# Kernel optimization log

Hardware: AMD Instinct MI355X
Metric: run time of the kernel (lower is better)

Reference implementation:

```python
import jax, jax.numpy as jnp
import numpy as np

D_MODEL = 256
NUM_HEADS = 8
HEAD_DIM = D_MODEL // NUM_HEADS


def setup_inputs() -> dict:
    key = jax.random.key(0)
    ks = jax.random.split(key, 16)
    B, C, H, W = 2, D_MODEL, 64, 64
    s = 0.02
    inp = {
        "query_feat": jax.random.normal(ks[0], (B, C, H, W), jnp.float32),
        "lateral_feat": jax.random.normal(ks[1], (B, C, H, W), jnp.float32),
        # 1x1 convs == per-pixel linear layers: weight (out, in), bias (out,)
        "Wq": jax.random.normal(ks[2], (C, C), jnp.float32) * s,
        "bq": jnp.zeros((C,), jnp.float32),
        "Wk": jax.random.normal(ks[3], (C, C), jnp.float32) * s,
        "bk": jnp.zeros((C,), jnp.float32),
        "Wv": jax.random.normal(ks[4], (C, C), jnp.float32) * s,
        "bv": jnp.zeros((C,), jnp.float32),
        "Wo": jax.random.normal(ks[5], (C, C), jnp.float32) * s,
        "bo": jnp.zeros((C,), jnp.float32),
        "W1": jax.random.normal(ks[6], (4 * C, C), jnp.float32) * s,
        "b1": jnp.zeros((4 * C,), jnp.float32),
        "W2": jax.random.normal(ks[7], (C, 4 * C), jnp.float32) * s,
        "b2": jnp.zeros((C,), jnp.float32),
    }
    return inp


def reference(query_feat, lateral_feat, Wq, bq, Wk, bk, Wv, bv, Wo, bo, W1, b1, W2, b2):
    B, C, H, W = query_feat.shape
    N = H * W
    h, d = NUM_HEADS, HEAD_DIM
    scale = d ** -0.5

    # (B,C,H,W) -> (B,N,C) tokens
    xq = query_feat.reshape(B, C, N).transpose(0, 2, 1)
    xl = lateral_feat.reshape(B, C, N).transpose(0, 2, 1)

    # 1x1-conv projections = dense per-token linear
    Q = (xq @ Wq.T + bq).reshape(B, N, h, d).transpose(0, 2, 1, 3)  # (B,h,N,d)
    K = (xl @ Wk.T + bk).reshape(B, N, h, d).transpose(0, 2, 1, 3)
    V = (xl @ Wv.T + bv).reshape(B, N, h, d).transpose(0, 2, 1, 3)

    scores = jnp.einsum("bhqd,bhkd->bhqk", Q, K) * scale  # (B,h,N,N)
    attn = jax.nn.softmax(scores, axis=-1)  # dropout = identity at inference
    out = jnp.einsum("bhqk,bhkd->bhqd", attn, V)  # (B,h,N,d)

    out = out.transpose(0, 2, 1, 3).reshape(B, N, C)  # (B,N,C)
    out = out @ Wo.T + bo
    out = out.transpose(0, 2, 1).reshape(B, C, H, W)
    out = out + query_feat  # residual

    # MLP on channels (1x1 convs + exact GELU)
    t = out.reshape(B, C, N).transpose(0, 2, 1)  # (B,N,C)
    hdn = jax.nn.gelu(t @ W1.T + b1, approximate=False)  # (B,N,4C)
    mlp = (hdn @ W2.T + b2).transpose(0, 2, 1).reshape(B, C, H, W)
    return out + mlp
```

## Files before the change

### kernel.cpp

```cpp
#include <hip/hip_runtime.h>
#include <math.h>

namespace {

constexpr int kB  = 2;
constexpr int kC  = 256;
constexpr int kN  = 4096;
constexpr int kHD = 32;
constexpr int kC4 = 1024;

typedef __attribute__((ext_vector_type(8))) short bf16x8;
typedef __attribute__((ext_vector_type(4))) float f32x4;
typedef __attribute__((ext_vector_type(16))) float f32x16;

__device__ __forceinline__ float gelu_exact(float x) {
  return 0.5f * x * (1.0f + erff(x * 0.70710678118654752f));
}

__device__ __forceinline__ unsigned short f2bf(float x) {
  unsigned u = __builtin_bit_cast(unsigned, x);
  u += 0x7FFFu + ((u >> 16) & 1u);
  return (unsigned short)(u >> 16);
}

__device__ __forceinline__ float bf2f(unsigned short us) {
  return __builtin_bit_cast(float, (unsigned)us << 16);
}

__device__ __forceinline__ float exp2_hw(float x) {
#if __has_builtin(__builtin_amdgcn_exp2f)
  return __builtin_amdgcn_exp2f(x);
#else
  float r;
  asm("v_exp_f32 %0, %1\n\ts_nop 1" : "=v"(r) : "v"(x));
  return r;
#endif
}

__device__ __forceinline__ unsigned cvt_pk_bf16(float lo, float hi) {
  unsigned r;
  asm("v_cvt_pk_bf16_f32 %0, %1, %2" : "=v"(r) : "v"(lo), "v"(hi));
  return r;
}

__global__ __launch_bounds__(256)
void convert_all(const float* __restrict__ qfeat, const float* __restrict__ lfeat,
                 const float* __restrict__ Wq, const float* __restrict__ Wk,
                 const float* __restrict__ Wv, const float* __restrict__ Wo,
                 const float* __restrict__ W1, const float* __restrict__ W2,
                 unsigned short* __restrict__ qtok, unsigned short* __restrict__ ltok,
                 unsigned short* __restrict__ wbf)
{
  __shared__ float Lds[32][36];
  const int z = blockIdx.z;
  const int t = threadIdx.x;
  if (z < 4) {
    const float* src = (z < kB) ? qfeat : lfeat;
    unsigned short* dst = (z < kB) ? qtok : ltok;
    const int b = z & 1;
    src += (size_t)b * kC * kN;
    dst += (size_t)b * kN * kC;
    const int n0 = blockIdx.x * 32, c0 = blockIdx.y * 32;
    const int r = t >> 3, q4 = (t & 7) * 4;
    {
      const float4 v = *(const float4*)&src[(size_t)(c0 + r) * kN + n0 + q4];
      Lds[r][q4 + 0] = v.x; Lds[r][q4 + 1] = v.y; Lds[r][q4 + 2] = v.z; Lds[r][q4 + 3] = v.w;
    }
    __syncthreads();
    ushort4 p;
    p.x = f2bf(Lds[q4 + 0][r]); p.y = f2bf(Lds[q4 + 1][r]);
    p.z = f2bf(Lds[q4 + 2][r]); p.w = f2bf(Lds[q4 + 3][r]);
    *(ushort4*)&dst[(size_t)(n0 + r) * kC + c0 + q4] = p;
  } else {
    const int wi = blockIdx.y * 128 + blockIdx.x;
    if (wi >= 768) return;
    const int i4 = wi * 1024 + t * 4;
    const float* s; int base;
    if      (i4 < 65536)  { s = Wq; base = 0; }
    else if (i4 < 131072) { s = Wk; base = 65536; }
    else if (i4 < 196608) { s = Wv; base = 131072; }
    else if (i4 < 262144) { s = Wo; base = 196608; }
    else if (i4 < 524288) { s = W1; base = 262144; }
    else                  { s = W2; base = 524288; }
    const float4 v = *(const float4*)&s[i4 - base];
    ushort4 p;
    p.x = f2bf(v.x); p.y = f2bf(v.y); p.z = f2bf(v.z); p.w = f2bf(v.w);
    *(ushort4*)&wbf[i4] = p;
  }
}

__global__ __launch_bounds__(256)
void gemm_qkv(const unsigned short* __restrict__ wbf,
              const unsigned short* __restrict__ qtok,
              const unsigned short* __restrict__ ltok,
              const float* __restrict__ bq, const float* __restrict__ bk,
              const float* __restrict__ bv,
              unsigned short* __restrict__ qout, unsigned short* __restrict__ kout,
              unsigned short* __restrict__ vout, float qscale)
{
  __shared__ unsigned short Wlds[2][64 * 64];
  __shared__ unsigned short Xlds[2][64 * 64];

  const int z = blockIdx.z;
  const bool isQ = blockIdx.y < 4;
  const int m0 = (isQ ? blockIdx.y : blockIdx.y - 4) * 64;
  const unsigned short* Wb = isQ ? wbf : (wbf + 65536);
  const unsigned short* Xt = (isQ ? qtok : ltok) + (size_t)z * kN * kC;

  const int t = threadIdx.x;
  const int w = t >> 6, l = t & 63;
  const int r = l & 15, g = l >> 4;
  const int wm = w >> 1, wn = w & 1;
  const int n0 = blockIdx.x * 64;

  const int rw = t >> 3;
  const int sw = (t & 7) ^ (rw & 7);
  const unsigned short* wsrc = Wb + (size_t)(m0 + rw) * kC + sw * 8;
  const unsigned short* xsrc = Xt + (size_t)(n0 + rw) * kC + sw * 8;

  f32x4 acc[2][2];
#pragma unroll
  for (int i = 0; i < 2; ++i)
#pragma unroll
    for (int j = 0; j < 2; ++j) acc[i][j] = {0.f, 0.f, 0.f, 0.f};

  bf16x8 wrg[2], xrg[2];
#pragma unroll
  for (int j = 0; j < 2; ++j) {
    wrg[j] = *(const bf16x8*)(wsrc + (size_t)(32 * j) * kC);
    xrg[j] = *(const bf16x8*)(xsrc + (size_t)(32 * j) * kC);
  }

  for (int it = 0; it < 4; ++it) {
    unsigned short* wl = &Wlds[it & 1][0];
    unsigned short* xl = &Xlds[it & 1][0];
    *(bf16x8*)((char*)wl + t * 16)         = wrg[0];
    *(bf16x8*)((char*)wl + (256 + t) * 16) = wrg[1];
    *(bf16x8*)((char*)xl + t * 16)         = xrg[0];
    *(bf16x8*)((char*)xl + (256 + t) * 16) = xrg[1];
    if (it + 1 < 4) {
      const int ko = (it + 1) * 64;
#pragma unroll
      for (int j = 0; j < 2; ++j) {
        wrg[j] = *(const bf16x8*)(wsrc + (size_t)(32 * j) * kC + ko);
        xrg[j] = *(const bf16x8*)(xsrc + (size_t)(32 * j) * kC + ko);
      }
    }
    __syncthreads();
#pragma unroll
    for (int kc = 0; kc < 2; ++kc) {
      const int sl = ((kc * 4 + g) ^ (r & 7)) * 16;
      bf16x8 a0 = *(const bf16x8*)((const char*)wl + (wm * 32 + r) * 128 + sl);
      bf16x8 a1 = *(const bf16x8*)((const char*)wl + (wm * 32 + 16 + r) * 128 + sl);
      bf16x8 b0 = *(const bf16x8*)((const char*)xl + (wn * 32 + r) * 128 + sl);
      bf16x8 b1 = *(const bf16x8*)((const char*)xl + (wn * 32 + 16 + r) * 128 + sl);
      acc[0][0] = __builtin_amdgcn_mfma_f32_16x16x32_bf16(a0, b0, acc[0][0], 0, 0, 0);
      acc[0][1] = __builtin_amdgcn_mfma_f32_16x16x32_bf16(a0, b1, acc[0][1], 0, 0, 0);
      acc[1][0] = __builtin_amdgcn_mfma_f32_16x16x32_bf16(a1, b0, acc[1][0], 0, 0, 0);
      acc[1][1] = __builtin_amdgcn_mfma_f32_16x16x32_bf16(a1, b1, acc[1][1], 0, 0, 0);
    }
  }

#pragma unroll
  for (int f = 0; f < 2; ++f) {
    const int mb = m0 + wm * 32 + f * 16 + 4 * g;
    const float* bp = isQ ? (bq + mb) : (mb < 256 ? (bk + mb) : (bv + mb - 256));
    const float4 b4 = *(const float4*)bp;
    const float os = isQ ? qscale : 1.0f;
#pragma unroll
    for (int fn = 0; fn < 2; ++fn) {
      const int n = n0 + wn * 32 + fn * 16 + r;
      float v[4];
      v[0] = (acc[f][fn][0] + b4.x) * os; v[1] = (acc[f][fn][1] + b4.y) * os;
      v[2] = (acc[f][fn][2] + b4.z) * os; v[3] = (acc[f][fn][3] + b4.w) * os;
      if (isQ) {
        unsigned short* Yt = qout + (size_t)z * kN * kC;
        ushort4 pk;
        pk.x = f2bf(v[0]); pk.y = f2bf(v[1]); pk.z = f2bf(v[2]); pk.w = f2bf(v[3]);
        *(ushort4*)&Yt[(size_t)n * kC + mb] = pk;
      } else if (mb < 256) {
        unsigned short* Yt = kout + (size_t)z * kN * kC;
        ushort4 pk;
        pk.x = f2bf(v[0]); pk.y = f2bf(v[1]); pk.z = f2bf(v[2]); pk.w = f2bf(v[3]);
        *(ushort4*)&Yt[(size_t)n * kC + mb] = pk;
      } else {
        unsigned short* Yc = vout + (size_t)z * kC * kN;
#pragma unroll
        for (int q = 0; q < 4; ++q) Yc[(size_t)(mb - 256 + q) * kN + n] = f2bf(v[q]);
      }
    }
  }
}

template <int EPI, bool GELU, bool RES>
__global__ __launch_bounds__(256)
void gemm_mfma(const unsigned short* __restrict__ Wbf,
               const unsigned short* __restrict__ Xtok,
               const float* __restrict__ bias, const float* __restrict__ res,
               void* __restrict__ Y1, void* __restrict__ Y2,
               int M, int Nn, int K, float oscale)
{
  __shared__ unsigned short Wlds[2][64 * 64];
  __shared__ unsigned short Xlds[2][64 * 64];

  const int z = blockIdx.z;
  Xtok += (size_t)z * Nn * K;

  const int t = threadIdx.x;
  const int w = t >> 6, l = t & 63;
  const int r = l & 15, g = l >> 4;
  const int wm = w >> 1, wn = w & 1;
  const int m0 = blockIdx.y * 64, n0 = blockIdx.x * 64;

  const int rw = t >> 3;
  const int sw = (t & 7) ^ (rw & 7);
  const unsigned short* wsrc = Wbf + (size_t)(m0 + rw) * K + sw * 8;
  const unsigned short* xsrc = Xtok + (size_t)(n0 + rw) * K + sw * 8;

  f32x4 acc[2][2];
#pragma unroll
  for (int i = 0; i < 2; ++i)
#pragma unroll
    for (int j = 0; j < 2; ++j) acc[i][j] = {0.f, 0.f, 0.f, 0.f};

  bf16x8 wrg[2], xrg[2];
#pragma unroll
  for (int j = 0; j < 2; ++j) {
    wrg[j] = *(const bf16x8*)(wsrc + (size_t)(32 * j) * K);
    xrg[j] = *(const bf16x8*)(xsrc + (size_t)(32 * j) * K);
  }

  const int nit = K >> 6;
  for (int it = 0; it < nit; ++it) {
    unsigned short* wl = &Wlds[it & 1][0];
    unsigned short* xl = &Xlds[it & 1][0];
    *(bf16x8*)((char*)wl + t * 16)         = wrg[0];
    *(bf16x8*)((char*)wl + (256 + t) * 16) = wrg[1];
    *(bf16x8*)((char*)xl + t * 16)         = xrg[0];
    *(bf16x8*)((char*)xl + (256 + t) * 16) = xrg[1];
    if (it + 1 < nit) {
      const int ko = (it + 1) * 64;
#pragma unroll
      for (int j = 0; j < 2; ++j) {
        wrg[j] = *(const bf16x8*)(wsrc + (size_t)(32 * j) * K + ko);
        xrg[j] = *(const bf16x8*)(xsrc + (size_t)(32 * j) * K + ko);
      }
    }
    __syncthreads();
#pragma unroll
    for (int kc = 0; kc < 2; ++kc) {
      const int sl = ((kc * 4 + g) ^ (r & 7)) * 16;
      bf16x8 a0 = *(const bf16x8*)((const char*)wl + (wm * 32 + r) * 128 + sl);
      bf16x8 a1 = *(const bf16x8*)((const char*)wl + (wm * 32 + 16 + r) * 128 + sl);
      bf16x8 b0 = *(const bf16x8*)((const char*)xl + (wn * 32 + r) * 128 + sl);
      bf16x8 b1 = *(const bf16x8*)((const char*)xl + (wn * 32 + 16 + r) * 128 + sl);
      acc[0][0] = __builtin_amdgcn_mfma_f32_16x16x32_bf16(a0, b0, acc[0][0], 0, 0, 0);
      acc[0][1] = __builtin_amdgcn_mfma_f32_16x16x32_bf16(a0, b1, acc[0][1], 0, 0, 0);
      acc[1][0] = __builtin_amdgcn_mfma_f32_16x16x32_bf16(a1, b0, acc[1][0], 0, 0, 0);
      acc[1][1] = __builtin_amdgcn_mfma_f32_16x16x32_bf16(a1, b1, acc[1][1], 0, 0, 0);
    }
  }

#pragma unroll
  for (int f = 0; f < 2; ++f) {
    const int mb = m0 + wm * 32 + f * 16 + 4 * g;
    const float4 b4 = *(const float4*)&bias[mb];
#pragma unroll
    for (int fn = 0; fn < 2; ++fn) {
      const int n = n0 + wn * 32 + fn * 16 + r;
      float v[4];
      v[0] = (acc[f][fn][0] + b4.x) * oscale; v[1] = (acc[f][fn][1] + b4.y) * oscale;
      v[2] = (acc[f][fn][2] + b4.z) * oscale; v[3] = (acc[f][fn][3] + b4.w) * oscale;
      if (GELU) {
#pragma unroll
        for (int q = 0; q < 4; ++q) v[q] = gelu_exact(v[q]);
      }
      if (RES) {
#pragma unroll
        for (int q = 0; q < 4; ++q)
          v[q] += res[(size_t)z * M * Nn + (size_t)(mb + q) * Nn + n];
      }
      if constexpr (EPI == 7) {
        const unsigned short* Rt = (const unsigned short*)Y2 + (size_t)z * Nn * M;
        const ushort4 rr = *(const ushort4*)&Rt[(size_t)n * M + mb];
        v[0] += bf2f(rr.x); v[1] += bf2f(rr.y); v[2] += bf2f(rr.z); v[3] += bf2f(rr.w);
      }
      if constexpr (EPI == 1 || EPI == 7) {
        unsigned short* Yt = (unsigned short*)Y1 + (size_t)z * Nn * M;
        ushort4 pk;
        pk.x = f2bf(v[0]); pk.y = f2bf(v[1]); pk.z = f2bf(v[2]); pk.w = f2bf(v[3]);
        *(ushort4*)&Yt[(size_t)n * M + mb] = pk;
      }
      if constexpr (EPI == 6) {
        float* Yf = (float*)Y1 + (size_t)z * M * Nn;
        const unsigned short* Rt = (const unsigned short*)Y2 + (size_t)z * Nn * M;
#pragma unroll
        for (int q = 0; q < 4; ++q)
          Yf[(size_t)(mb + q) * Nn + n] = v[q] + bf2f(Rt[(size_t)n * M + mb + q]);
      }
    }
  }
}

__global__ __launch_bounds__(1024, 4)
void attn_mfma32(const unsigned short* __restrict__ Qbf,
                 const unsigned short* __restrict__ Kbf,
                 const unsigned short* __restrict__ Vbf,
                 unsigned short* __restrict__ Aout)
{
  __shared__ __attribute__((aligned(16))) char smem[65536];

  const int id = blockIdx.x;
  const int bh = id & 15;
  const int b = bh >> 3, hd = bh & 7;
  const int t = threadIdx.x;
  const int w = t >> 6, l = t & 63;
  const int r = l & 31, hi = l >> 5;
  const int qg = w >> 2, kh = w & 3;

  const unsigned short* Qb = Qbf + (size_t)b * kN * kC;
  const unsigned short* Kb = Kbf + (size_t)b * kN * kC;
  const unsigned short* Vb = Vbf + ((size_t)b * kC + hd * kHD) * kN;
  unsigned short* Ap = Aout + (size_t)b * kN * kC;

  const int q0 = (id >> 4) * 128 + qg * 32;

  const bf16x8 qf0 = *(const bf16x8*)&Qb[(size_t)(q0 + r) * kC + hd * kHD + hi * 8];
  const bf16x8 qf1 = *(const bf16x8*)&Qb[(size_t)(q0 + r) * kC + hd * kHD + 16 + hi * 8];

  const int tt = t & 255, qd = t >> 8;
  const unsigned short* ksrc = Kb + (size_t)(qd * 1024 + (tt >> 2)) * kC + hd * kHD + (tt & 3) * 8;
  const unsigned short* vsrc = Vb + (size_t)(tt >> 3) * kN + qd * 1024 + (tt & 7) * 8;
  char* kdst = smem + qd * 8192 + ((tt & 3) * 64 + ((tt >> 2) ^ (9 * (tt & 3)))) * 16;
  char* vdst = smem + qd * 8192 + 4096 + ((tt & 7) * 32 + ((tt >> 3) ^ (tt & 7))) * 16;

  int koff[2][2], voff[2][2];
#pragma unroll
  for (int ds = 0; ds < 2; ++ds)
#pragma unroll
    for (int tile = 0; tile < 2; ++tile) {
      const int c = 2 * ds + hi;
      koff[ds][tile] = kh * 8192 + (c * 64 + tile * 32 + (r ^ (9 * c))) * 16;
    }
#pragma unroll
  for (int ktile = 0; ktile < 2; ++ktile)
#pragma unroll
    for (int kc = 0; kc < 2; ++kc) {
      const int c = ktile * 4 + kc * 2 + hi;
      voff[ktile][kc] = kh * 8192 + 4096 + (c * 32 + (r ^ c)) * 16;
    }

  const f32x16 ZV = {0.f};
  f32x16 oA = ZV, oB = ZV;
  float lsum = 0.f;

  bf16x8 krg = *(const bf16x8*)ksrc;
  bf16x8 vrg = *(const bf16x8*)vsrc;

  for (int it = 0; it < 16; ++it) {
    const int bo = (it & 1) << 15;
    *(bf16x8*)(kdst + bo) = krg;
    *(bf16x8*)(vdst + bo) = vrg;
    if (it + 1 < 16) {
      krg = *(const bf16x8*)(ksrc + (size_t)(it + 1) * 64 * kC);
      vrg = *(const bf16x8*)(vsrc + (it + 1) * 64);
    }
    __syncthreads();

    bf16x8 ka00 = *(const bf16x8*)(smem + bo + koff[0][0]);
    bf16x8 ka10 = *(const bf16x8*)(smem + bo + koff[1][0]);
    bf16x8 ka01 = *(const bf16x8*)(smem + bo + koff[0][1]);
    bf16x8 ka11 = *(const bf16x8*)(smem + bo + koff[1][1]);
    __builtin_amdgcn_s_setprio(1);
    f32x16 s0 = __builtin_amdgcn_mfma_f32_32x32x16_bf16(ka00, qf0, ZV, 0, 0, 0);
    s0        = __builtin_amdgcn_mfma_f32_32x32x16_bf16(ka10, qf1, s0, 0, 0, 0);
    f32x16 s1 = __builtin_amdgcn_mfma_f32_32x32x16_bf16(ka01, qf0, ZV, 0, 0, 0);
    s1        = __builtin_amdgcn_mfma_f32_32x32x16_bf16(ka11, qf1, s1, 0, 0, 0);
    __builtin_amdgcn_s_setprio(0);

#pragma unroll
    for (int ktile = 0; ktile < 2; ++ktile) {
      const f32x16& sv = ktile ? s1 : s0;
      float pe[16];
#pragma unroll
      for (int j = 0; j < 16; ++j) pe[j] = exp2_hw(sv[j]);
      lsum += (((pe[0] + pe[1]) + (pe[2] + pe[3])) + ((pe[4] + pe[5]) + (pe[6] + pe[7])))
            + (((pe[8] + pe[9]) + (pe[10] + pe[11])) + ((pe[12] + pe[13]) + (pe[14] + pe[15])));
      const unsigned c0 = cvt_pk_bf16(pe[0], pe[1]),   c1 = cvt_pk_bf16(pe[2], pe[3]);
      const unsigned c2 = cvt_pk_bf16(pe[4], pe[5]),   c3 = cvt_pk_bf16(pe[6], pe[7]);
      const unsigned c4 = cvt_pk_bf16(pe[8], pe[9]),   c5 = cvt_pk_bf16(pe[10], pe[11]);
      const unsigned c6 = cvt_pk_bf16(pe[12], pe[13]), c7 = cvt_pk_bf16(pe[14], pe[15]);
      auto a02 = __builtin_amdgcn_permlane32_swap(c0, c2, false, false);
      auto a13 = __builtin_amdgcn_permlane32_swap(c1, c3, false, false);
      auto a46 = __builtin_amdgcn_permlane32_swap(c4, c6, false, false);
      auto a57 = __builtin_amdgcn_permlane32_swap(c5, c7, false, false);
      union { unsigned u[4]; bf16x8 v; } p0, p1;
      p0.u[0] = a02[0]; p0.u[1] = a13[0]; p0.u[2] = a02[1]; p0.u[3] = a13[1];
      p1.u[0] = a46[0]; p1.u[1] = a57[0]; p1.u[2] = a46[1]; p1.u[3] = a57[1];
      bf16x8 vf0 = *(const bf16x8*)(smem + bo + voff[ktile][0]);
      bf16x8 vf1 = *(const bf16x8*)(smem + bo + voff[ktile][1]);
      __builtin_amdgcn_s_setprio(1);
      oA = __builtin_amdgcn_mfma_f32_32x32x16_bf16(vf0, p0.v, oA, 0, 0, 0);
      oB = __builtin_amdgcn_mfma_f32_32x32x16_bf16(vf1, p1.v, oB, 0, 0, 0);
      __builtin_amdgcn_s_setprio(0);
    }
  }

  {
    auto pr = __builtin_amdgcn_permlane32_swap(
        __builtin_bit_cast(unsigned, lsum), __builtin_bit_cast(unsigned, lsum), false, false);
    lsum = __builtin_bit_cast(float, (unsigned)pr[0]) + __builtin_bit_cast(float, (unsigned)pr[1]);
  }
  float oS[16];
#pragma unroll
  for (int j = 0; j < 16; ++j) oS[j] = oA[j] + oB[j];

  float* Scr = (float*)smem;
  __syncthreads();
  if (kh != 0) {
    float* S = Scr + ((size_t)(qg * 3 + (kh - 1)) * 64 + l) * 17;
#pragma unroll
    for (int j = 0; j < 16; ++j) S[j] = oS[j];
    S[16] = lsum;
  }
  __syncthreads();
  if (kh == 0) {
#pragma unroll
    for (int p = 0; p < 3; ++p) {
      const float* S = Scr + ((size_t)(qg * 3 + p) * 64 + l) * 17;
#pragma unroll
      for (int j = 0; j < 16; ++j) oS[j] += S[j];
      lsum += S[16];
    }
    const float inv = 1.f / lsum;

    unsigned* T = (unsigned*)(Scr + (size_t)qg * 3 * 64 * 17);
#pragma unroll
    for (int p = 0; p < 8; ++p) {
      const int r2 = 4 * (p >> 1) + 2 * hi + (p & 1);
      T[r2 * 33 + r] = cvt_pk_bf16(oS[2 * p] * inv, oS[2 * p + 1] * inv);
    }
    unsigned v[8];
#pragma unroll
    for (int j = 0; j < 8; ++j) v[j] = T[(8 * hi + j) * 33 + r];
    unsigned short* outp = Ap + (size_t)(q0 + r) * kC + hd * kHD + hi * 16;
    uint4 w0{v[0], v[1], v[2], v[3]}, w1{v[4], v[5], v[6], v[7]};
    *(uint4*)outp = w0;
    *(uint4*)(outp + 8) = w1;
  }
}

}

extern "C" void kernel_launch(void* const* d_in, const int* in_sizes, int n_in,
                              void* d_out, int out_size, void* d_ws, size_t ws_size,
                              hipStream_t stream)
{
  const float* qfeat = (const float*)d_in[0];
  const float* lfeat = (const float*)d_in[1];
  const float* Wq = (const float*)d_in[2];
  const float* bq = (const float*)d_in[3];
  const float* Wk = (const float*)d_in[4];
  const float* bk = (const float*)d_in[5];
  const float* Wv = (const float*)d_in[6];
  const float* bv = (const float*)d_in[7];
  const float* Wo = (const float*)d_in[8];
  const float* bo = (const float*)d_in[9];
  const float* W1 = (const float*)d_in[10];
  const float* b1 = (const float*)d_in[11];
  const float* W2 = (const float*)d_in[12];
  const float* b2 = (const float*)d_in[13];
  float* out = (float*)d_out;
  (void)in_sizes; (void)n_in; (void)out_size; (void)ws_size;

  constexpr float kScaleLog2e = 0.25506970f;

  const size_t bcn = (size_t)kB * kC * kN;
  unsigned short* qtok   = (unsigned short*)d_ws;
  unsigned short* ltok   = qtok + bcn;
  unsigned short* wbf    = ltok + bcn;
  unsigned short* qbf    = wbf + 786432;
  unsigned short* kbf    = qbf + bcn;
  unsigned short* vbf    = kbf + bcn;
  unsigned short* atok   = vbf + bcn;
  unsigned short* owstok = atok + bcn;
  unsigned short* h1tok  = owstok + bcn;

  dim3 blk(256);

  convert_all<<<dim3(128, 8, 5), blk, 0, stream>>>(
      qfeat, lfeat, Wq, Wk, Wv, Wo, W1, W2, qtok, ltok, wbf);

  gemm_qkv<<<dim3(64, 12, 2), blk, 0, stream>>>(
      wbf, qtok, ltok, bq, bk, bv, qbf, kbf, vbf, kScaleLog2e);

  attn_mfma32<<<dim3(512), dim3(1024), 0, stream>>>(qbf, kbf, vbf, atok);

  gemm_mfma<7, false, false><<<dim3(64, 4, 2), blk, 0, stream>>>(
      wbf + 196608, atok, bo, nullptr, owstok, qtok, kC, kN, kC, 1.0f);
  gemm_mfma<1, true, false><<<dim3(64, 16, 2), blk, 0, stream>>>(
      wbf + 262144, owstok, b1, nullptr, h1tok, nullptr, kC4, kN, kC, 1.0f);
  gemm_mfma<6, false, false><<<dim3(64, 4, 2), blk, 0, stream>>>(
      wbf + 524288, h1tok, b2, nullptr, out, owstok, kC, kN, kC4, 1.0f);
}
```

Baseline: 101.0 us.

## Load K/V fragments directly from global memory in attention, halving block size

```diff
diff --git a/kernel.cpp b/kernel.cpp
--- a/kernel.cpp
+++ b/kernel.cpp
@@ -302,13 +302,13 @@
   }
 }
 
-__global__ __launch_bounds__(1024, 4)
-void attn_mfma32(const unsigned short* __restrict__ Qbf,
+__global__ __launch_bounds__(512, 4)
+void attn_direct(const unsigned short* __restrict__ Qbf,
                  const unsigned short* __restrict__ Kbf,
                  const unsigned short* __restrict__ Vbf,
                  unsigned short* __restrict__ Aout)
 {
-  __shared__ __attribute__((aligned(16))) char smem[65536];
+  __shared__ float Scr[2][3][64][17];
 
   const int id = blockIdx.x;
   const int bh = id & 15;
@@ -323,54 +323,30 @@
   const unsigned short* Vb = Vbf + ((size_t)b * kC + hd * kHD) * kN;
   unsigned short* Ap = Aout + (size_t)b * kN * kC;
 
-  const int q0 = (id >> 4) * 128 + qg * 32;
+  const int q0 = (id >> 4) * 64 + qg * 32;
 
   const bf16x8 qf0 = *(const bf16x8*)&Qb[(size_t)(q0 + r) * kC + hd * kHD + hi * 8];
   const bf16x8 qf1 = *(const bf16x8*)&Qb[(size_t)(q0 + r) * kC + hd * kHD + 16 + hi * 8];
 
-  const int tt = t & 255, qd = t >> 8;
-  const unsigned short* ksrc = Kb + (size_t)(qd * 1024 + (tt >> 2)) * kC + hd * kHD + (tt & 3) * 8;
-  const unsigned short* vsrc = Vb + (size_t)(tt >> 3) * kN + qd * 1024 + (tt & 7) * 8;
-  char* kdst = smem + qd * 8192 + ((tt & 3) * 64 + ((tt >> 2) ^ (9 * (tt & 3)))) * 16;
-  char* vdst = smem + qd * 8192 + 4096 + ((tt & 7) * 32 + ((tt >> 3) ^ (tt & 7))) * 16;
-
-  int koff[2][2], voff[2][2];
-#pragma unroll
-  for (int ds = 0; ds < 2; ++ds)
-#pragma unroll
-    for (int tile = 0; tile < 2; ++tile) {
-      const int c = 2 * ds + hi;
-      koff[ds][tile] = kh * 8192 + (c * 64 + tile * 32 + (r ^ (9 * c))) * 16;
-    }
-#pragma unroll
-  for (int ktile = 0; ktile < 2; ++ktile)
-#pragma unroll
-    for (int kc = 0; kc < 2; ++kc) {
-      const int c = ktile * 4 + kc * 2 + hi;
-      voff[ktile][kc] = kh * 8192 + 4096 + (c * 32 + (r ^ c)) * 16;
-    }
+  const unsigned short* kp0 = Kb + (size_t)(kh * 1024 + r) * kC + hd * kHD + hi * 8;
+  const unsigned short* kp1 = kp0 + (size_t)32 * kC;
+  const unsigned short* vp  = Vb + (size_t)r * kN + kh * 1024 + hi * 8;
 
   const f32x16 ZV = {0.f};
   f32x16 oA = ZV, oB = ZV;
   float lsum = 0.f;
 
-  bf16x8 krg = *(const bf16x8*)ksrc;
-  bf16x8 vrg = *(const bf16x8*)vsrc;
-
   for (int it = 0; it < 16; ++it) {
-    const int bo = (it & 1) << 15;
-    *(bf16x8*)(kdst + bo) = krg;
-    *(bf16x8*)(vdst + bo) = vrg;
-    if (it + 1 < 16) {
-      krg = *(const bf16x8*)(ksrc + (size_t)(it + 1) * 64 * kC);
-      vrg = *(const bf16x8*)(vsrc + (it + 1) * 64);
-    }
-    __syncthreads();
-
-    bf16x8 ka00 = *(const bf16x8*)(smem + bo + koff[0][0]);
-    bf16x8 ka10 = *(const bf16x8*)(smem + bo + koff[1][0]);
-    bf16x8 ka01 = *(const bf16x8*)(smem + bo + koff[0][1]);
-    bf16x8 ka11 = *(const bf16x8*)(smem + bo + koff[1][1]);
+    bf16x8 ka00 = *(const bf16x8*)(kp0);
+    bf16x8 ka10 = *(const bf16x8*)(kp0 + 16);
+    bf16x8 ka01 = *(const bf16x8*)(kp1);
+    bf16x8 ka11 = *(const bf16x8*)(kp1 + 16);
+    bf16x8 vf00 = *(const bf16x8*)(vp);
+    bf16x8 vf01 = *(const bf16x8*)(vp + 16);
+    bf16x8 vf10 = *(const bf16x8*)(vp + 32);
+    bf16x8 vf11 = *(const bf16x8*)(vp + 48);
+    kp0 += (size_t)64 * kC; kp1 += (size_t)64 * kC; vp += 64;
+
     __builtin_amdgcn_s_setprio(1);
     f32x16 s0 = __builtin_amdgcn_mfma_f32_32x32x16_bf16(ka00, qf0, ZV, 0, 0, 0);
     s0        = __builtin_amdgcn_mfma_f32_32x32x16_bf16(ka10, qf1, s0, 0, 0, 0);
@@ -397,11 +373,9 @@
       union { unsigned u[4]; bf16x8 v; } p0, p1;
       p0.u[0] = a02[0]; p0.u[1] = a13[0]; p0.u[2] = a02[1]; p0.u[3] = a13[1];
       p1.u[0] = a46[0]; p1.u[1] = a57[0]; p1.u[2] = a46[1]; p1.u[3] = a57[1];
-      bf16x8 vf0 = *(const bf16x8*)(smem + bo + voff[ktile][0]);
-      bf16x8 vf1 = *(const bf16x8*)(smem + bo + voff[ktile][1]);
       __builtin_amdgcn_s_setprio(1);
-      oA = __builtin_amdgcn_mfma_f32_32x32x16_bf16(vf0, p0.v, oA, 0, 0, 0);
-      oB = __builtin_amdgcn_mfma_f32_32x32x16_bf16(vf1, p1.v, oB, 0, 0, 0);
+      oA = __builtin_amdgcn_mfma_f32_32x32x16_bf16(ktile ? vf10 : vf00, p0.v, oA, 0, 0, 0);
+      oB = __builtin_amdgcn_mfma_f32_32x32x16_bf16(ktile ? vf11 : vf01, p1.v, oB, 0, 0, 0);
       __builtin_amdgcn_s_setprio(0);
     }
   }
@@ -415,10 +389,8 @@
 #pragma unroll
   for (int j = 0; j < 16; ++j) oS[j] = oA[j] + oB[j];
 
-  float* Scr = (float*)smem;
-  __syncthreads();
   if (kh != 0) {
-    float* S = Scr + ((size_t)(qg * 3 + (kh - 1)) * 64 + l) * 17;
+    float* S = &Scr[qg][kh - 1][l][0];
 #pragma unroll
     for (int j = 0; j < 16; ++j) S[j] = oS[j];
     S[16] = lsum;
@@ -427,14 +399,14 @@
   if (kh == 0) {
 #pragma unroll
     for (int p = 0; p < 3; ++p) {
-      const float* S = Scr + ((size_t)(qg * 3 + p) * 64 + l) * 17;
+      const float* S = &Scr[qg][p][l][0];
 #pragma unroll
       for (int j = 0; j < 16; ++j) oS[j] += S[j];
       lsum += S[16];
     }
     const float inv = 1.f / lsum;
 
-    unsigned* T = (unsigned*)(Scr + (size_t)qg * 3 * 64 * 17);
+    unsigned* T = (unsigned*)&Scr[qg][0][0][0];
 #pragma unroll
     for (int p = 0; p < 8; ++p) {
       const int r2 = 4 * (p >> 1) + 2 * hi + (p & 1);
@@ -494,7 +466,7 @@
   gemm_qkv<<<dim3(64, 12, 2), blk, 0, stream>>>(
       wbf, qtok, ltok, bq, bk, bv, qbf, kbf, vbf, kScaleLog2e);
 
-  attn_mfma32<<<dim3(512), dim3(1024), 0, stream>>>(qbf, kbf, vbf, atok);
+  attn_direct<<<dim3(1024), dim3(512), 0, stream>>>(qbf, kbf, vbf, atok);
 
   gemm_mfma<7, false, false><<<dim3(64, 4, 2), blk, 0, stream>>>(
       wbf + 196608, atok, bo, nullptr, owstok, qtok, kC, kN, kC, 1.0f);
```

After: 167.9 us. +66.3%, slower.
